# Kernel tuning notes

Hardware: AMD Instinct MI355X
Metric: run time of the kernel (lower is better)

The kernel has to match this reference:

```python
import jax, jax.numpy as jnp
import numpy as np
import math

NUM_HEADS = 16
HEAD_DIM = 64
EMBED = NUM_HEADS * HEAD_DIM  # 1024
T_FEAT = 128


def setup_inputs() -> dict:
    key = jax.random.key(0)
    ks = jax.random.split(key, 9)
    B, S = 4, 2048
    x = jax.random.normal(ks[0], (B, S, EMBED), dtype=jnp.float32)
    time_enc = jax.random.normal(ks[1], (B, T_FEAT), dtype=jnp.float32)
    s = 1.0 / math.sqrt(EMBED)
    Wq = jax.random.normal(ks[2], (EMBED, EMBED), dtype=jnp.float32) * s
    Wk = jax.random.normal(ks[3], (EMBED, EMBED), dtype=jnp.float32) * s
    Wv = jax.random.normal(ks[4], (EMBED, EMBED), dtype=jnp.float32) * s
    Wo = jax.random.normal(ks[5], (EMBED, EMBED), dtype=jnp.float32) * s
    bo = jnp.zeros((EMBED,), dtype=jnp.float32)
    Wt = jax.random.normal(ks[6], (T_FEAT, NUM_HEADS), dtype=jnp.float32) * (1.0 / math.sqrt(T_FEAT))
    bt = jnp.zeros((NUM_HEADS,), dtype=jnp.float32)
    return {"x": x, "time_enc": time_enc, "Wq": Wq, "Wk": Wk, "Wv": Wv,
            "Wo": Wo, "bo": bo, "Wt": Wt, "bt": bt}


def reference(x, time_enc, Wq, Wk, Wv, Wo, bo, Wt, bt):
    B, S, E = x.shape
    H, D = NUM_HEADS, HEAD_DIM
    scale = 1.0 / math.sqrt(D)
    # projections (no bias on q/k/v, bias on out)
    q = (x @ Wq).reshape(B, S, H, D).transpose(0, 2, 1, 3)  # [B,H,S,D]
    k = (x @ Wk).reshape(B, S, H, D).transpose(0, 2, 1, 3)
    v = (x @ Wv).reshape(B, S, H, D).transpose(0, 2, 1, 3)
    scores = jnp.einsum('bhqd,bhkd->bhqk', q, k) * scale
    # time-dependent per-head weighting (softmax over heads)
    time_weights = jax.nn.softmax(time_enc @ Wt + bt)  # [B,H]
    scores = scores * time_weights.reshape(B, H, 1, 1)
    attn = jax.nn.softmax(scores, axis=-1)
    out = jnp.einsum('bhqk,bhkd->bhqd', attn, v)
    out = out.transpose(0, 2, 1, 3).reshape(B, S, E)
    return out @ Wo + bo
```

## Files before the change

kernel.cpp:

```cpp
#include <hip/hip_runtime.h>
#include <cstdint>
#include <cstddef>

#define EMB   1024
#define NH    16
#define HD    64
#define SEQ   2048
#define NB    4
#define MROWS 8192

typedef short short8 __attribute__((ext_vector_type(8)));
typedef float floatx4 __attribute__((ext_vector_type(4)));

__device__ __forceinline__ unsigned short f2bf(float f) {
  return (unsigned short)((__float_as_uint(f) + 0x8000u) >> 16);
}

__device__ __forceinline__ void load16_lds(const unsigned short* g, unsigned short* l) {
  __builtin_amdgcn_global_load_lds((const __attribute__((address_space(1))) void*)g,
                                   (__attribute__((address_space(3))) void*)l, 16, 0, 0);
}

__global__ void time_weights_kernel(const float* __restrict__ te, const float* __restrict__ Wt,
                                    const float* __restrict__ bt, float* __restrict__ tw) {
  int t = threadIdx.x;
  int b = t >> 4, h = t & 15;
  float acc = bt[h];
  for (int i = 0; i < 128; i++) acc += te[b * 128 + i] * Wt[i * 16 + h];
  float m = acc;
  for (int off = 1; off < 16; off <<= 1) m = fmaxf(m, __shfl_xor(m, off, 16));
  float e = __expf(acc - m);
  float s = e;
  for (int off = 1; off < 16; off <<= 1) s += __shfl_xor(s, off, 16);
  tw[t] = (e / s) * 0.125f * 1.4426950408889634f;
}

__global__ void convert_x_kernel(const float4* __restrict__ x, unsigned short* __restrict__ out) {
  int i = blockIdx.x * blockDim.x + threadIdx.x;
  float4 v = x[i];
  unsigned int u0 = __float_as_uint(v.x) + 0x8000u, u1 = __float_as_uint(v.y) + 0x8000u;
  unsigned int u2 = __float_as_uint(v.z) + 0x8000u, u3 = __float_as_uint(v.w) + 0x8000u;
  uint2 p;
  p.x = (u0 >> 16) | (u1 & 0xffff0000u);
  p.y = (u2 >> 16) | (u3 & 0xffff0000u);
  *(uint2*)&out[(size_t)i * 4] = p;
}

__global__ void transpose_convert4_kernel(const float* __restrict__ Wq, const float* __restrict__ Wk,
                                          const float* __restrict__ Wv, const float* __restrict__ Wo,
                                          unsigned short* __restrict__ wqkvt, unsigned short* __restrict__ wot) {
  __shared__ float tile[32][33];
  int z = blockIdx.z;
  const float* W = (z == 0) ? Wq : (z == 1) ? Wk : (z == 2) ? Wv : Wo;
  unsigned short* out = (z < 3) ? (wqkvt + (size_t)z * EMB * EMB) : wot;
  int k0 = blockIdx.x * 32;
  int n0 = blockIdx.y * 32;
  int tx = threadIdx.x;
  int ty = threadIdx.y;
#pragma unroll
  for (int i = 0; i < 4; i++) {
    int k = ty + i * 8;
    tile[k][tx] = W[(size_t)(k0 + k) * EMB + n0 + tx];
  }
  __syncthreads();
#pragma unroll
  for (int i = 0; i < 4; i++) {
    int n = ty + i * 8;
    out[(size_t)(n0 + n) * EMB + k0 + tx] = f2bf(tile[tx][n]);
  }
}

template <int EPI>
__global__ __launch_bounds__(512, 2) void gemm_kernel(
    const unsigned short* __restrict__ A, const unsigned short* __restrict__ Bt,
    unsigned short* __restrict__ qo, unsigned short* __restrict__ ko, unsigned short* __restrict__ vto,
    float* __restrict__ outf, const float* __restrict__ bias, const float* __restrict__ tw) {
  __shared__ unsigned short ldsu[32768];

  const int tid = threadIdx.x;
  const int lane = tid & 63, wid = tid >> 6;
  const int quad = lane >> 4, l16 = lane & 15;
  const int wm = wid >> 2, wn = wid & 3;

  const int gx = gridDim.x;
  const int nwg = gx * gridDim.y;
  const int fid = blockIdx.y * gx + blockIdx.x;
  const int swzid = (fid & 7) * (nwg >> 3) + (fid >> 3);
  const int m0 = (swzid / gx) * 256;
  const int n0 = (swzid % gx) * 256;

  const int trow = tid >> 2;
  const int sw = (((tid & 3) ^ ((tid >> 2) & 3) ^ ((tid >> 4) & 3))) * 8;
  const unsigned short* gA0 = A + (size_t)(m0 + trow) * 1024 + sw;
  const unsigned short* gA1 = A + (size_t)(m0 + 128 + trow) * 1024 + sw;
  const unsigned short* gB0 = Bt + (size_t)(n0 + trow) * 1024 + sw;
  const unsigned short* gB1 = Bt + (size_t)(n0 + 128 + trow) * 1024 + sw;
  unsigned short* lds_w = ldsu + (wid << 9);

  const int swl = (l16 & 3) ^ (l16 >> 2);
  const int foff = (quad ^ swl) * 8;
  const int abase = (wm * 128 + l16) * 32 + foff;
  const int bbase = 8192 + (wn * 64 + l16) * 32 + foff;

  floatx4 acc[8][4];
#pragma unroll
  for (int mi = 0; mi < 8; mi++)
#pragma unroll
    for (int ni = 0; ni < 4; ni++)
#pragma unroll
      for (int r = 0; r < 4; r++) acc[mi][ni][r] = 0.f;

  load16_lds(gA0, lds_w);
  load16_lds(gA1, lds_w + 4096);
  load16_lds(gB0, lds_w + 8192);
  load16_lds(gB1, lds_w + 12288);

  for (int t = 0; t < 32; ++t) {
    const int cur = (t & 1) << 14;
    const int nxt = ((t + 1) & 1) << 14;
    const int kc = ((t + 1) & 31) * 32;
    load16_lds(gA0 + kc, lds_w + nxt);
    load16_lds(gA1 + kc, lds_w + nxt + 4096);
    load16_lds(gB0 + kc, lds_w + nxt + 8192);
    load16_lds(gB1 + kc, lds_w + nxt + 12288);
    asm volatile("s_waitcnt vmcnt(4)" ::: "memory");
    asm volatile("s_barrier" ::: "memory");

    short8 af[8], bf[4];
#pragma unroll
    for (int mi = 0; mi < 8; mi++) af[mi] = *(const short8*)&ldsu[cur + abase + mi * 512];
#pragma unroll
    for (int ni = 0; ni < 4; ni++) bf[ni] = *(const short8*)&ldsu[cur + bbase + ni * 512];
    __builtin_amdgcn_s_setprio(1);
#pragma unroll
    for (int mi = 0; mi < 8; mi++)
#pragma unroll
      for (int ni = 0; ni < 4; ni++)
        acc[mi][ni] = __builtin_amdgcn_mfma_f32_16x16x32_bf16(af[mi], bf[ni], acc[mi][ni], 0, 0, 0);
    __builtin_amdgcn_s_setprio(0);
    asm volatile("s_barrier" ::: "memory");
  }
  asm volatile("s_waitcnt vmcnt(0)" ::: "memory");

  if (EPI == 1) {
#pragma unroll
    for (int mi = 0; mi < 8; mi++)
#pragma unroll
      for (int ni = 0; ni < 4; ni++) {
        const int n = n0 + wn * 64 + ni * 16 + l16;
        const float bs = bias[n];
        const int mb = m0 + wm * 128 + mi * 16 + quad * 4;
#pragma unroll
        for (int r = 0; r < 4; r++)
          outf[(size_t)(mb + r) * EMB + n] = acc[mi][ni][r] + bs;
      }
  } else {
    const int proj = n0 >> 10;
    const int b = m0 >> 11;
    const int hw = ((n0 + wn * 64) >> 6) & 15;
    const size_t bh = (size_t)b * NH + hw;
    const int mbase = m0 + wm * 128;
    if (proj == 0) {
      const float tws = tw[bh];
#pragma unroll
      for (int mi = 0; mi < 8; mi++) {
        const int s = ((mbase + mi * 16) & 2047) + quad * 4;
#pragma unroll
        for (int ni = 0; ni < 4; ni++) {
          const int d = ni * 16 + l16;
          unsigned short* qp = qo + (bh * SEQ + s) * HD + d;
#pragma unroll
          for (int r = 0; r < 4; r++) qp[(size_t)r * HD] = f2bf(acc[mi][ni][r] * tws);
        }
      }
    } else if (proj == 1) {
#pragma unroll
      for (int mi = 0; mi < 8; mi++) {
        const int s = ((mbase + mi * 16) & 2047) + quad * 4;
#pragma unroll
        for (int ni = 0; ni < 4; ni++) {
          const int d = ni * 16 + l16;
          unsigned short* kp = ko + (bh * SEQ + s) * HD + d;
#pragma unroll
          for (int r = 0; r < 4; r++) kp[(size_t)r * HD] = f2bf(acc[mi][ni][r]);
        }
      }
    } else {
#pragma unroll
      for (int mi = 0; mi < 8; mi++) {
        const int s = ((mbase + mi * 16) & 2047) + quad * 4;
#pragma unroll
        for (int ni = 0; ni < 4; ni++) {
          const int d = ni * 16 + l16;
          unsigned int u0 = __float_as_uint(acc[mi][ni][0]) + 0x8000u;
          unsigned int u1 = __float_as_uint(acc[mi][ni][1]) + 0x8000u;
          unsigned int u2 = __float_as_uint(acc[mi][ni][2]) + 0x8000u;
          unsigned int u3 = __float_as_uint(acc[mi][ni][3]) + 0x8000u;
          uint2 w;
          w.x = (u0 >> 16) | (u1 & 0xffff0000u);
          w.y = (u2 >> 16) | (u3 & 0xffff0000u);
          *(uint2*)&vto[(bh * HD + d) * SEQ + s] = w;
        }
      }
    }
  }
}

__global__ __launch_bounds__(256, 4) void attn_kernel(
    const unsigned short* __restrict__ qg, const unsigned short* __restrict__ kg,
    const unsigned short* __restrict__ vtg, unsigned short* __restrict__ aog) {
  __shared__ unsigned short Ks[64 * 64];
  __shared__ unsigned short Vs[64 * 64];
  __shared__ unsigned short Ps[4 * 2048];

  int tid = threadIdx.x;
  int lane = tid & 63, wid = tid >> 6;
  int quad = lane >> 4, l16 = lane & 15, l7 = lane & 7;
  int qt = blockIdx.x, h = blockIdx.y, b = blockIdx.z;
  int bh = b * NH + h;
  const unsigned short* qbase = qg + (size_t)bh * SEQ * HD + (size_t)qt * 128 * HD;
  const unsigned short* kbase = kg + (size_t)bh * SEQ * HD;
  const unsigned short* vbase = vtg + (size_t)bh * HD * SEQ;

  short8 b_q[2][2];
#pragma unroll
  for (int mi = 0; mi < 2; mi++)
#pragma unroll
    for (int kk = 0; kk < 2; kk++)
      b_q[mi][kk] = *(const short8*)&qbase[(wid * 32 + mi * 16 + l16) * 64 + kk * 32 + quad * 8];

  const unsigned short* gK[2];
  const unsigned short* gV[2];
  unsigned short* lK[2];
  unsigned short* lV[2];
#pragma unroll
  for (int c = 0; c < 2; c++) {
    int row = wid * 16 + c * 8 + (lane >> 3);
    int gcol = ((lane & 7) ^ (row & 7)) * 8;
    gK[c] = kbase + row * 64 + gcol;
    gV[c] = vbase + (size_t)row * SEQ + gcol;
    lK[c] = &Ks[(wid * 16 + c * 8) * 64];
    lV[c] = &Vs[(wid * 16 + c * 8) * 64];
  }

  int pg[2];
#pragma unroll
  for (int i = 0; i < 2; i++) pg[i] = l16 * 64 + (((i * 4 + quad) ^ l7) * 8);

  int wbase = wid * 2048;
  int chunkx = l16 & 14;
  int pwa[4];
#pragma unroll
  for (int ni = 0; ni < 4; ni++)
    pwa[ni] = wbase + l16 * 64 + (((ni * 4 + quad) ^ chunkx) * 4);
  int pra[2];
#pragma unroll
  for (int kk2 = 0; kk2 < 2; kk2++)
    pra[kk2] = wbase + l16 * 64 + (((kk2 * 8 + quad * 2) ^ chunkx) * 4);

  floatx4 O[4][2];
  float lsum[2] = {0.f, 0.f};
#pragma unroll
  for (int di = 0; di < 4; di++)
#pragma unroll
    for (int mi = 0; mi < 2; mi++)
#pragma unroll
      for (int r = 0; r < 4; r++) O[di][mi][r] = 0.f;

  for (int kb = 0; kb < 32; kb++) {
    __syncthreads();
#pragma unroll
    for (int c = 0; c < 2; c++) {
      load16_lds(gK[c] + kb * 4096, lK[c]);
      load16_lds(gV[c] + kb * 64, lV[c]);
    }
    asm volatile("s_waitcnt vmcnt(0) lgkmcnt(0)" ::: "memory");
    __syncthreads();

    floatx4 st[4][2];
#pragma unroll
    for (int ni = 0; ni < 4; ni++)
#pragma unroll
      for (int mi = 0; mi < 2; mi++)
#pragma unroll
        for (int r = 0; r < 4; r++) st[ni][mi][r] = 0.f;
#pragma unroll
    for (int kk = 0; kk < 2; kk++)
#pragma unroll
      for (int ni = 0; ni < 4; ni++) {
        short8 a_k = *(const short8*)&Ks[ni * 1024 + pg[kk]];
#pragma unroll
        for (int mi = 0; mi < 2; mi++)
          st[ni][mi] = __builtin_amdgcn_mfma_f32_16x16x32_bf16(a_k, b_q[mi][kk], st[ni][mi], 0, 0, 0);
      }

#pragma unroll
    for (int mi = 0; mi < 2; mi++)
#pragma unroll
      for (int ni = 0; ni < 4; ni++) {
        float p0 = __builtin_amdgcn_exp2f(st[ni][mi][0]);
        float p1 = __builtin_amdgcn_exp2f(st[ni][mi][1]);
        float p2 = __builtin_amdgcn_exp2f(st[ni][mi][2]);
        float p3 = __builtin_amdgcn_exp2f(st[ni][mi][3]);
        lsum[mi] += (p0 + p1) + (p2 + p3);
        unsigned int u0 = __float_as_uint(p0) + 0x8000u, u1 = __float_as_uint(p1) + 0x8000u;
        unsigned int u2 = __float_as_uint(p2) + 0x8000u, u3 = __float_as_uint(p3) + 0x8000u;
        uint2 w;
        w.x = (u0 >> 16) | (u1 & 0xffff0000u);
        w.y = (u2 >> 16) | (u3 & 0xffff0000u);
        *(uint2*)&Ps[pwa[ni] + mi * 1024] = w;
      }
    asm volatile("s_waitcnt lgkmcnt(0)" ::: "memory");

#pragma unroll
    for (int kk2 = 0; kk2 < 2; kk2++) {
      short8 av[4], bp[2];
#pragma unroll
      for (int di = 0; di < 4; di++)
        av[di] = *(const short8*)&Vs[di * 1024 + pg[kk2]];
#pragma unroll
      for (int mi = 0; mi < 2; mi++)
        bp[mi] = *(const short8*)&Ps[pra[kk2] + mi * 1024];
#pragma unroll
      for (int di = 0; di < 4; di++)
#pragma unroll
        for (int mi = 0; mi < 2; mi++)
          O[di][mi] = __builtin_amdgcn_mfma_f32_16x16x32_bf16(av[di], bp[mi], O[di][mi], 0, 0, 0);
    }
  }

  float inv[2];
#pragma unroll
  for (int mi = 0; mi < 2; mi++) {
    lsum[mi] += __shfl_xor(lsum[mi], 16);
    lsum[mi] += __shfl_xor(lsum[mi], 32);
    inv[mi] = 1.0f / lsum[mi];
  }

#pragma unroll
  for (int mi = 0; mi < 2; mi++) {
    int s = qt * 128 + wid * 32 + mi * 16 + l16;
    size_t rowbase = ((size_t)(b * SEQ + s) * NH + h) * HD;
#pragma unroll
    for (int di = 0; di < 4; di++) {
      unsigned int u0 = __float_as_uint(O[di][mi][0] * inv[mi]) + 0x8000u;
      unsigned int u1 = __float_as_uint(O[di][mi][1] * inv[mi]) + 0x8000u;
      unsigned int u2 = __float_as_uint(O[di][mi][2] * inv[mi]) + 0x8000u;
      unsigned int u3 = __float_as_uint(O[di][mi][3] * inv[mi]) + 0x8000u;
      uint2 w;
      w.x = (u0 >> 16) | (u1 & 0xffff0000u);
      w.y = (u2 >> 16) | (u3 & 0xffff0000u);
      *(uint2*)&aog[rowbase + di * 16 + quad * 4] = w;
    }
  }
}

extern "C" void kernel_launch(void* const* d_in, const int* in_sizes, int n_in,
                              void* d_out, int out_size, void* d_ws, size_t ws_size,
                              hipStream_t stream) {
  (void)in_sizes; (void)n_in; (void)out_size; (void)ws_size;
  const float* x  = (const float*)d_in[0];
  const float* te = (const float*)d_in[1];
  const float* Wq = (const float*)d_in[2];
  const float* Wk = (const float*)d_in[3];
  const float* Wv = (const float*)d_in[4];
  const float* Wo = (const float*)d_in[5];
  const float* bo = (const float*)d_in[6];
  const float* Wt = (const float*)d_in[7];
  const float* bt = (const float*)d_in[8];
  float* out = (float*)d_out;

  char* ws = (char*)d_ws;
  size_t off = 0;
  auto carve = [&](size_t bytes) -> void* {
    void* p = ws + off;
    off += (bytes + 255) & ~(size_t)255;
    return p;
  };
  float* twb            = (float*)carve(64 * sizeof(float));
  unsigned short* xb    = (unsigned short*)carve((size_t)MROWS * EMB * 2);
  unsigned short* wqkvt = (unsigned short*)carve((size_t)3 * EMB * EMB * 2);
  unsigned short* wot   = (unsigned short*)carve((size_t)EMB * EMB * 2);
  unsigned short* vtb   = (unsigned short*)carve((size_t)MROWS * EMB * 2);
  unsigned short* qb    = (unsigned short*)d_out;
  unsigned short* kb    = (unsigned short*)d_out + (size_t)MROWS * EMB;
  unsigned short* ao    = xb;

  time_weights_kernel<<<dim3(1), dim3(64), 0, stream>>>(te, Wt, bt, twb);
  convert_x_kernel<<<dim3(8192), dim3(256), 0, stream>>>((const float4*)x, xb);
  transpose_convert4_kernel<<<dim3(32, 32, 4), dim3(32, 8), 0, stream>>>(Wq, Wk, Wv, Wo, wqkvt, wot);
  gemm_kernel<0><<<dim3(12, 32), dim3(512), 0, stream>>>(xb, wqkvt, qb, kb, vtb, nullptr, nullptr, twb);
  attn_kernel<<<dim3(16, NH, NB), dim3(256), 0, stream>>>(qb, kb, vtb, ao);
  gemm_kernel<1><<<dim3(4, 32), dim3(512), 0, stream>>>(ao, wot, nullptr, nullptr, nullptr, out, bo, nullptr);
}
```

Before: 302.3 us.

## Prefetch attention K/V tiles via registers and rework GEMM load mapping and epilogue order

```diff
diff --git a/kernel.cpp b/kernel.cpp
--- a/kernel.cpp
+++ b/kernel.cpp
@@ -89,13 +89,14 @@
   const int m0 = (swzid / gx) * 256;
   const int n0 = (swzid % gx) * 256;
 
-  const int trow = tid >> 2;
-  const int sw = (((tid & 3) ^ ((tid >> 2) & 3) ^ ((tid >> 4) & 3))) * 8;
-  const unsigned short* gA0 = A + (size_t)(m0 + trow) * 1024 + sw;
-  const unsigned short* gA1 = A + (size_t)(m0 + 128 + trow) * 1024 + sw;
-  const unsigned short* gB0 = Bt + (size_t)(n0 + trow) * 1024 + sw;
-  const unsigned short* gB1 = Bt + (size_t)(n0 + 128 + trow) * 1024 + sw;
-  unsigned short* lds_w = ldsu + (wid << 9);
+  const int sw8 = (((lane & 3) ^ ((lane >> 2) & 3) ^ ((lane >> 4) & 3))) * 8;
+  const int rowA = wid * 32 + (lane >> 2);
+  const unsigned short* gA0 = A + (size_t)(m0 + rowA) * 1024 + sw8;
+  const unsigned short* gA1 = gA0 + (size_t)16 * 1024;
+  const unsigned short* gB0 = Bt + (size_t)(n0 + rowA) * 1024 + sw8;
+  const unsigned short* gB1 = gB0 + (size_t)16 * 1024;
+  unsigned short* lwA = ldsu + wid * 1024;
+  unsigned short* lwB = ldsu + 8192 + wid * 1024;
 
   const int swl = (l16 & 3) ^ (l16 >> 2);
   const int foff = (quad ^ swl) * 8;
@@ -110,19 +111,19 @@
 #pragma unroll
       for (int r = 0; r < 4; r++) acc[mi][ni][r] = 0.f;
 
-  load16_lds(gA0, lds_w);
-  load16_lds(gA1, lds_w + 4096);
-  load16_lds(gB0, lds_w + 8192);
-  load16_lds(gB1, lds_w + 12288);
+  load16_lds(gA0, lwA);
+  load16_lds(gA1, lwA + 512);
+  load16_lds(gB0, lwB);
+  load16_lds(gB1, lwB + 512);
 
   for (int t = 0; t < 32; ++t) {
     const int cur = (t & 1) << 14;
     const int nxt = ((t + 1) & 1) << 14;
     const int kc = ((t + 1) & 31) * 32;
-    load16_lds(gA0 + kc, lds_w + nxt);
-    load16_lds(gA1 + kc, lds_w + nxt + 4096);
-    load16_lds(gB0 + kc, lds_w + nxt + 8192);
-    load16_lds(gB1 + kc, lds_w + nxt + 12288);
+    load16_lds(gA0 + kc, lwA + nxt);
+    load16_lds(gA1 + kc, lwA + nxt + 512);
+    load16_lds(gB0 + kc, lwB + nxt);
+    load16_lds(gB1 + kc, lwB + nxt + 512);
     asm volatile("s_waitcnt vmcnt(4)" ::: "memory");
     asm volatile("s_barrier" ::: "memory");
 
@@ -131,43 +132,43 @@
     for (int mi = 0; mi < 8; mi++) af[mi] = *(const short8*)&ldsu[cur + abase + mi * 512];
 #pragma unroll
     for (int ni = 0; ni < 4; ni++) bf[ni] = *(const short8*)&ldsu[cur + bbase + ni * 512];
-    __builtin_amdgcn_s_setprio(1);
 #pragma unroll
     for (int mi = 0; mi < 8; mi++)
 #pragma unroll
       for (int ni = 0; ni < 4; ni++)
         acc[mi][ni] = __builtin_amdgcn_mfma_f32_16x16x32_bf16(af[mi], bf[ni], acc[mi][ni], 0, 0, 0);
-    __builtin_amdgcn_s_setprio(0);
     asm volatile("s_barrier" ::: "memory");
   }
   asm volatile("s_waitcnt vmcnt(0)" ::: "memory");
 
   if (EPI == 1) {
 #pragma unroll
-    for (int mi = 0; mi < 8; mi++)
-#pragma unroll
-      for (int ni = 0; ni < 4; ni++) {
-        const int n = n0 + wn * 64 + ni * 16 + l16;
-        const float bs = bias[n];
+    for (int ni = 0; ni < 4; ni++) {
+      const int n = n0 + wn * 64 + ni * 16 + l16;
+      const float bs = bias[n];
+#pragma unroll
+      for (int mi = 0; mi < 8; mi++) {
         const int mb = m0 + wm * 128 + mi * 16 + quad * 4;
 #pragma unroll
         for (int r = 0; r < 4; r++)
           outf[(size_t)(mb + r) * EMB + n] = acc[mi][ni][r] + bs;
       }
+    }
   } else {
     const int proj = n0 >> 10;
     const int b = m0 >> 11;
-    const int hw = ((n0 + wn * 64) >> 6) & 15;
-    const size_t bh = (size_t)b * NH + hw;
-    const int mbase = m0 + wm * 128;
+    const int sb = (m0 & 2047) + wm * 128 + quad * 4;
     if (proj == 0) {
-      const float tws = tw[bh];
-#pragma unroll
-      for (int mi = 0; mi < 8; mi++) {
-        const int s = ((mbase + mi * 16) & 2047) + quad * 4;
-#pragma unroll
-        for (int ni = 0; ni < 4; ni++) {
-          const int d = ni * 16 + l16;
+#pragma unroll
+      for (int ni = 0; ni < 4; ni++) {
+        const int nb = n0 + wn * 64 + ni * 16;
+        const int hh = (nb >> 6) & 15;
+        const int d = (nb & 63) + l16;
+        const size_t bh = (size_t)b * NH + hh;
+        const float tws = tw[bh];
+#pragma unroll
+        for (int mi = 0; mi < 8; mi++) {
+          const int s = sb + mi * 16;
           unsigned short* qp = qo + (bh * SEQ + s) * HD + d;
 #pragma unroll
           for (int r = 0; r < 4; r++) qp[(size_t)r * HD] = f2bf(acc[mi][ni][r] * tws);
@@ -175,11 +176,14 @@
       }
     } else if (proj == 1) {
 #pragma unroll
-      for (int mi = 0; mi < 8; mi++) {
-        const int s = ((mbase + mi * 16) & 2047) + quad * 4;
-#pragma unroll
-        for (int ni = 0; ni < 4; ni++) {
-          const int d = ni * 16 + l16;
+      for (int ni = 0; ni < 4; ni++) {
+        const int nb = n0 + wn * 64 + ni * 16;
+        const int hh = (nb >> 6) & 15;
+        const int d = (nb & 63) + l16;
+        const size_t bh = (size_t)b * NH + hh;
+#pragma unroll
+        for (int mi = 0; mi < 8; mi++) {
+          const int s = sb + mi * 16;
           unsigned short* kp = ko + (bh * SEQ + s) * HD + d;
 #pragma unroll
           for (int r = 0; r < 4; r++) kp[(size_t)r * HD] = f2bf(acc[mi][ni][r]);
@@ -187,11 +191,14 @@
       }
     } else {
 #pragma unroll
-      for (int mi = 0; mi < 8; mi++) {
-        const int s = ((mbase + mi * 16) & 2047) + quad * 4;
-#pragma unroll
-        for (int ni = 0; ni < 4; ni++) {
-          const int d = ni * 16 + l16;
+      for (int ni = 0; ni < 4; ni++) {
+        const int nb = n0 + wn * 64 + ni * 16;
+        const int hh = (nb >> 6) & 15;
+        const int d = (nb & 63) + l16;
+        const size_t bh = (size_t)b * NH + hh;
+#pragma unroll
+        for (int mi = 0; mi < 8; mi++) {
+          const int s = sb + mi * 16;
           unsigned int u0 = __float_as_uint(acc[mi][ni][0]) + 0x8000u;
           unsigned int u1 = __float_as_uint(acc[mi][ni][1]) + 0x8000u;
           unsigned int u2 = __float_as_uint(acc[mi][ni][2]) + 0x8000u;
@@ -267,15 +274,19 @@
 #pragma unroll
       for (int r = 0; r < 4; r++) O[di][mi][r] = 0.f;
 
+  load16_lds(gK[0], lK[0]);
+  load16_lds(gK[1], lK[1]);
+  load16_lds(gV[0], lV[0]);
+  load16_lds(gV[1], lV[1]);
+  asm volatile("s_waitcnt vmcnt(0)" ::: "memory");
+  __syncthreads();
+
   for (int kb = 0; kb < 32; kb++) {
-    __syncthreads();
-#pragma unroll
-    for (int c = 0; c < 2; c++) {
-      load16_lds(gK[c] + kb * 4096, lK[c]);
-      load16_lds(gV[c] + kb * 64, lV[c]);
-    }
-    asm volatile("s_waitcnt vmcnt(0) lgkmcnt(0)" ::: "memory");
-    __syncthreads();
+    const int kn = (kb + 1) & 31;
+    short8 kreg0 = *(const short8*)(gK[0] + kn * 4096);
+    short8 kreg1 = *(const short8*)(gK[1] + kn * 4096);
+    short8 vreg0 = *(const short8*)(gV[0] + kn * 64);
+    short8 vreg1 = *(const short8*)(gV[1] + kn * 64);
 
     floatx4 st[4][2];
 #pragma unroll
@@ -327,6 +338,13 @@
         for (int mi = 0; mi < 2; mi++)
           O[di][mi] = __builtin_amdgcn_mfma_f32_16x16x32_bf16(av[di], bp[mi], O[di][mi], 0, 0, 0);
     }
+
+    __syncthreads();
+    *(short8*)&lK[0][lane * 8] = kreg0;
+    *(short8*)&lK[1][lane * 8] = kreg1;
+    *(short8*)&lV[0][lane * 8] = vreg0;
+    *(short8*)&lV[1][lane * 8] = vreg1;
+    __syncthreads();
   }
 
   float inv[2];
```

Result: no change. 301.9 us (-0.1%).
